# Optimization experiments

Hardware: AMD Instinct MI355X
Metric: run time of the kernel (lower is better)

The kernel has to match this reference:

```python
import jax, jax.numpy as jnp
import numpy as np

EPS = 1e-6      # l2_norm / denom clamp eps
BN_EPS = 1e-5   # BatchNorm eps


def _l2norm(x):
    # torch.norm(p=2, dim=-2, keepdim=True).clamp_min(eps)
    n = jnp.sqrt(jnp.sum(x * x, axis=-2, keepdims=True))
    return x / jnp.maximum(n, EPS)


def setup_inputs() -> dict:
    key = jax.random.key(0)
    ks = jax.random.split(key, 9)
    B, Cin_each, Co, H, W = 4, 256, 256, 128, 128
    Cq = Co // 8  # in_places // scale
    Cin = 4 * Cin_each
    return {
        "s5": jax.random.normal(ks[0], (B, Cin_each, H, W), jnp.float32),
        "s4": jax.random.normal(ks[1], (B, Cin_each, H, W), jnp.float32),
        "s3": jax.random.normal(ks[2], (B, Cin_each, H, W), jnp.float32),
        "s2": jax.random.normal(ks[3], (B, Cin_each, H, W), jnp.float32),
        # ConvBnRelu: 1x1 conv (no bias) + BN affine params
        "w_conv": jax.random.normal(ks[4], (Co, Cin), jnp.float32) * 0.03,
        "bn_gamma": jnp.ones((Co,), jnp.float32),
        "bn_beta": jnp.zeros((Co,), jnp.float32),
        # Attention 1x1 convs (with bias)
        "wq": jax.random.normal(ks[5], (Cq, Co), jnp.float32) * 0.06,
        "bq": jnp.zeros((Cq,), jnp.float32),
        "wk": jax.random.normal(ks[6], (Cq, Co), jnp.float32) * 0.06,
        "bk": jnp.zeros((Cq,), jnp.float32),
        "wv": jax.random.normal(ks[7], (Co, Co), jnp.float32) * 0.06,
        "bv": jnp.zeros((Co,), jnp.float32),
        # gamma is Parameter(zeros(1)) in the source; set nonzero so the
        # attention branch contributes to the output for kernel testing.
        "gamma": jnp.array(0.5, jnp.float32),
    }


def reference(s5, s4, s3, s2, w_conv, bn_gamma, bn_beta,
              wq, bq, wk, bk, wv, bv, gamma):
    # --- ConvBnRelu (1x1 conv, train-mode BN, ReLU) ---
    fcat = jnp.concatenate([s5, s4, s3, s2], axis=1)            # [B, 4C, H, W]
    x = jnp.einsum('oc,bchw->bohw', w_conv, fcat)               # 1x1 conv
    mu = x.mean(axis=(0, 2, 3), keepdims=True)
    var = x.var(axis=(0, 2, 3), keepdims=True)                  # biased, as torch BN
    x = (x - mu) / jnp.sqrt(var + BN_EPS)
    x = x * bn_gamma[None, :, None, None] + bn_beta[None, :, None, None]
    feat = jax.nn.relu(x)                                       # [B, C, H, W]

    # --- linear Attention (L2-norm QK, KV trick, no softmax) ---
    B, C, H, W = feat.shape
    N = H * W
    X = feat.reshape(B, C, N)
    Q = jnp.einsum('qc,bcn->bqn', wq, X) + bq[None, :, None]    # [B, Cq, N]
    K = jnp.einsum('qc,bcn->bqn', wk, X) + bk[None, :, None]    # [B, Cq, N]
    V = jnp.einsum('oc,bcn->bon', wv, X) + bv[None, :, None]    # [B, C, N]

    Qn = _l2norm(Q)                                             # norm over channel dim
    Kn = _l2norm(K)

    # denom: N + Q . sum_n K
    e = jnp.einsum('bqn,bq->bn', Qn, Kn.sum(axis=-1))           # [B, N]
    tailor = 1.0 / jnp.maximum(jnp.asarray(N, Qn.dtype) + e, 1e-6)

    # KV trick: [B, Cq, C] then project back through Q
    matrix = jnp.einsum('bqn,bcn->bqc', Kn, V)                  # [B, Cq, C]
    matrix_sum = V.sum(axis=-1)[:, :, None] + \
        jnp.einsum('bqn,bqc->bcn', Qn, matrix)                  # [B, C, N]

    weight_value = matrix_sum * tailor[:, None, :]              # [B, C, N]
    out = gamma * weight_value.reshape(B, C, H, W)
    out = jnp.nan_to_num(out, nan=0.0, posinf=1.0, neginf=-1.0)

    return out + feat
```

## Files before the change

### kernel.cpp

```cpp
#include <hip/hip_runtime.h>

#define B_   4
#define CO   256
#define CIN  1024
#define CQ   32
#define HN   16384
#define NPIX 65536
#define NTOT ((size_t)B_ * CO * HN)

typedef unsigned short ushort_t;
typedef __attribute__((ext_vector_type(8))) short bf16x8;
typedef __attribute__((ext_vector_type(4))) float f32x4;

__device__ __forceinline__ unsigned bf16pair(float x, float y) {
    unsigned xu = __float_as_uint(x), yu = __float_as_uint(y);
    unsigned xr = (xu + 0x7FFFu + ((xu >> 16) & 1u)) >> 16;
    unsigned yr = (yu + 0x7FFFu + ((yu >> 16) & 1u)) >> 16;
    return xr | (yr << 16);
}
__device__ __forceinline__ ushort_t bf16of(float x) {
    unsigned u = __float_as_uint(x);
    return (ushort_t)((u + 0x7FFFu + ((u >> 16) & 1u)) >> 16);
}
__device__ __forceinline__ float bf2f(ushort_t h) {
    return __uint_as_float(((unsigned)h) << 16);
}
__device__ __forceinline__ void unpack8(uint4 u, float* f) {
    f[0] = __uint_as_float(u.x << 16); f[1] = __uint_as_float(u.x & 0xffff0000u);
    f[2] = __uint_as_float(u.y << 16); f[3] = __uint_as_float(u.y & 0xffff0000u);
    f[4] = __uint_as_float(u.z << 16); f[5] = __uint_as_float(u.z & 0xffff0000u);
    f[6] = __uint_as_float(u.w << 16); f[7] = __uint_as_float(u.w & 0xffff0000u);
}
__device__ __forceinline__ void async16(void* lds, const void* g) {
    __builtin_amdgcn_global_load_lds(
        (const __attribute__((address_space(1))) void*)g,
        (__attribute__((address_space(3))) void*)lds, 16, 0, 0);
}

__global__ __launch_bounds__(256) void wcvt(
    const float* __restrict__ w, const float* __restrict__ wq,
    const float* __restrict__ wk, const float* __restrict__ wv,
    ushort_t* __restrict__ w_bf, ushort_t* __restrict__ wqk_bf,
    ushort_t* __restrict__ wv_bf)
{
    int i = blockIdx.x * 256 + threadIdx.x;
    if (i < 262144) {
        w_bf[i] = bf16of(w[i]);
    } else if (i < 278528) {
        int l = i - 262144; int row = l >> 8, col = l & 255;
        float v = (row < 32) ? wq[row * 256 + col] : wk[(row - 32) * 256 + col];
        wqk_bf[l] = bf16of(v);
    } else {
        int l = i - 278528;
        wv_bf[l] = bf16of(wv[l]);
    }
}

__global__ __launch_bounds__(256) void conv_mfma3(
    const float* __restrict__ s5, const float* __restrict__ s4,
    const float* __restrict__ s3, const float* __restrict__ s2,
    const ushort_t* __restrict__ w_bf, ushort_t* __restrict__ xb)
{
    __shared__ ushort_t Aw[2][128 * 32];
    __shared__ ushort_t Bn[2][128 * 40];
    const int o0 = blockIdx.x * 128;
    const int n0 = blockIdx.y * 128;
    const int b  = blockIdx.z;
    const int tid = threadIdx.x;
    const int wave = tid >> 6, lane = tid & 63, l15 = lane & 15, quad = lane >> 4;
    const int wm = wave & 1, wn = wave >> 1;
    const int n_st = tid & 127;
    const int kqb  = tid >> 7;
    const int bswz = ((n_st >> 3) & 3) << 1;
    f32x4 acc[4][4] = {};
    float v[4][4];

    auto loadB = [&](int k0) {
        const float* base = (k0 < 256) ? s5 : (k0 < 512) ? s4
                          : (k0 < 768) ? s3 : s2;
        const float* sp = base + ((size_t)b * 256 + (k0 & 255)) * HN + n0 + n_st;
        #pragma unroll
        for (int i = 0; i < 4; ++i) {
            const float* cp = sp + (size_t)(kqb + 2 * i) * 4 * HN;
            #pragma unroll
            for (int j = 0; j < 4; ++j) v[i][j] = cp[(size_t)j * HN];
        }
    };
    auto storeB = [&](int bi) {
        ushort_t* Bp = Bn[bi];
        #pragma unroll
        for (int i = 0; i < 4; ++i) {
            int pos = (kqb + 2 * i) ^ bswz;
            uint2 u = make_uint2(bf16pair(v[i][0], v[i][1]),
                                 bf16pair(v[i][2], v[i][3]));
            *(uint2*)&Bp[n_st * 40 + pos * 4] = u;
        }
    };
    auto issueA = [&](int k0, int bi) {
        #pragma unroll
        for (int r = 0; r < 2; ++r) {
            int row  = r * 64 + wave * 16;
            int orow = row + (lane >> 2);
            const ushort_t* g = w_bf + (size_t)(o0 + orow) * CIN + k0
                                + (((lane & 3) ^ ((orow >> 1) & 3)) << 3);
            async16(&Aw[bi][row * 32], g);
        }
    };

    issueA(0, 0);
    loadB(0);
    storeB(0);

    int buf = 0;
    for (int k0 = 0; k0 < CIN; k0 += 32) {
        __syncthreads();
        const bool more = (k0 + 32 < CIN);
        if (more) { issueA(k0 + 32, buf ^ 1); loadB(k0 + 32); }
        bf16x8 af[4], bfv[4];
        #pragma unroll
        for (int tm = 0; tm < 4; ++tm) {
            int orow = wm * 64 + tm * 16 + l15;
            int pos  = quad ^ ((orow >> 1) & 3);
            af[tm] = *(const bf16x8*)&Aw[buf][orow * 32 + pos * 8];
        }
        #pragma unroll
        for (int tn = 0; tn < 4; ++tn) {
            int nl = wn * 64 + tn * 16 + l15;
            int p0 = (2 * quad) ^ (((nl >> 3) & 3) << 1);
            bfv[tn] = *(const bf16x8*)&Bn[buf][nl * 40 + p0 * 4];
        }
        #pragma unroll
        for (int tm = 0; tm < 4; ++tm)
            #pragma unroll
            for (int tn = 0; tn < 4; ++tn)
                acc[tm][tn] = __builtin_amdgcn_mfma_f32_16x16x32_bf16(
                    af[tm], bfv[tn], acc[tm][tn], 0, 0, 0);
        if (more) storeB(buf ^ 1);
        buf ^= 1;
    }
    #pragma unroll
    for (int tm = 0; tm < 4; ++tm)
        #pragma unroll
        for (int r = 0; r < 4; ++r) {
            int o = o0 + wm * 64 + tm * 16 + quad * 4 + r;
            size_t base = ((size_t)b * CO + o) * HN + n0;
            #pragma unroll
            for (int tn = 0; tn < 4; ++tn)
                xb[base + wn * 64 + tn * 16 + l15] = bf16of(acc[tm][tn][r]);
        }
}

__global__ __launch_bounds__(256) void bn_stats(
    const ushort_t* __restrict__ xb, float* __restrict__ accum)
{
    const int o = blockIdx.x, seg = blockIdx.y, tid = threadIdx.x;
    const int wave = tid >> 6, lane = tid & 63;
    float s = 0.f, ss = 0.f;
    for (int b = 0; b < B_; ++b) {
        const ushort_t* p = xb + ((size_t)(b * CO + o)) * HN + seg * 2048 + tid * 8;
        uint4 u = *(const uint4*)p;
        float f[8]; unpack8(u, f);
        #pragma unroll
        for (int j = 0; j < 8; ++j) { s += f[j]; ss += f[j] * f[j]; }
    }
    #pragma unroll
    for (int m = 1; m < 64; m <<= 1) { s += __shfl_xor(s, m); ss += __shfl_xor(ss, m); }
    __shared__ float shs[4], shss[4];
    if (lane == 0) { shs[wave] = s; shss[wave] = ss; }
    __syncthreads();
    if (tid == 0) {
        atomicAdd(&accum[o],       shs[0] + shs[1] + shs[2] + shs[3]);
        atomicAdd(&accum[256 + o], shss[0] + shss[1] + shss[2] + shss[3]);
    }
}

__global__ __launch_bounds__(256) void bn_finalize(
    const float* __restrict__ accum, const float* __restrict__ g,
    const float* __restrict__ bt, float* __restrict__ scale,
    float* __restrict__ shift)
{
    int o = threadIdx.x;
    float mu  = accum[o] / (float)NPIX;
    float var = accum[256 + o] / (float)NPIX - mu * mu;
    float sc  = g[o] * rsqrtf(var + 1e-5f);
    scale[o] = sc;
    shift[o] = bt[o] - mu * sc;
}

__global__ __launch_bounds__(256) void bnrelu_t(
    const ushort_t* __restrict__ xb, const float* __restrict__ scale,
    const float* __restrict__ shift, ushort_t* __restrict__ featT)
{
    __shared__ ushort_t sh[64 * 68];
    const int hn0 = blockIdx.x * 64, c0 = blockIdx.y * 64, b = blockIdx.z;
    const int tid = threadIdx.x;
    {
        int cl = tid >> 2, seg = tid & 3;
        float sc = scale[c0 + cl], sf = shift[c0 + cl];
        const ushort_t* src = xb + ((size_t)(b * CO + c0 + cl)) * HN + hn0 + seg * 16;
        #pragma unroll
        for (int h = 0; h < 2; ++h) {
            uint4 u = *(const uint4*)(src + h * 8);
            float f[8]; unpack8(u, f);
            #pragma unroll
            for (int j = 0; j < 8; ++j) {
                float v = fmaxf(fmaf(sc, f[j], sf), 0.f);
                sh[(seg * 16 + h * 8 + j) * 68 + cl] = bf16of(v);
            }
        }
    }
    __syncthreads();
    {
        int nl = tid >> 2, seg = tid & 3;
        size_t gn = (size_t)b * HN + hn0 + nl;
        ushort_t* dst = featT + gn * CO + c0 + seg * 16;
        #pragma unroll
        for (int j = 0; j < 4; ++j)
            *(uint2*)(dst + j * 4) = *(const uint2*)&sh[nl * 68 + seg * 16 + j * 4];
    }
}

__global__ __launch_bounds__(256) void qk_mfma(
    const ushort_t* __restrict__ featT, const ushort_t* __restrict__ wqk_bf,
    const float* __restrict__ bq, const float* __restrict__ bk,
    ushort_t* __restrict__ Qt, ushort_t* __restrict__ KtT,
    float* __restrict__ Ksum)
{
    __shared__ ushort_t At[128 * 32];
    __shared__ ushort_t Bt[64 * 32];
    const int n0 = blockIdx.x * 128;
    const int b  = n0 >> 14;
    const int hn0 = n0 & 16383;
    const int tid = threadIdx.x;
    const int wave = tid >> 6, lane = tid & 63, l15 = lane & 15, quad = lane >> 4;
    const int nsub = (wave & 1) * 64;
    const int isK  = wave >> 1;
    f32x4 acc[4][2] = {};

    for (int k0 = 0; k0 < CO; k0 += 32) {
        #pragma unroll
        for (int r = 0; r < 2; ++r) {
            int row = r * 64 + wave * 16;
            const ushort_t* g = featT + (size_t)(n0 + row + (lane >> 2)) * CO
                                + k0 + (lane & 3) * 8;
            async16(&At[row * 32], g);
        }
        {
            int row = wave * 16;
            const ushort_t* g = wqk_bf + (size_t)(row + (lane >> 2)) * CO
                                + k0 + (lane & 3) * 8;
            async16(&Bt[row * 32], g);
        }
        __syncthreads();
        bf16x8 af[4], bfv[2];
        #pragma unroll
        for (int tm = 0; tm < 4; ++tm)
            af[tm] = *(const bf16x8*)&At[(nsub + tm * 16 + l15) * 32 + quad * 8];
        #pragma unroll
        for (int tc = 0; tc < 2; ++tc)
            bfv[tc] = *(const bf16x8*)&Bt[(isK * 32 + tc * 16 + l15) * 32 + quad * 8];
        #pragma unroll
        for (int tm = 0; tm < 4; ++tm)
            #pragma unroll
            for (int tc = 0; tc < 2; ++tc)
                acc[tm][tc] = __builtin_amdgcn_mfma_f32_16x16x32_bf16(
                    af[tm], bfv[tc], acc[tm][tc], 0, 0, 0);
        __syncthreads();
    }
    const float bias0 = isK ? bk[l15]      : bq[l15];
    const float bias1 = isK ? bk[16 + l15] : bq[16 + l15];
    float ks0 = 0.f, ks1 = 0.f;
    #pragma unroll
    for (int tm = 0; tm < 4; ++tm)
        #pragma unroll
        for (int r = 0; r < 4; ++r) {
            float v0 = acc[tm][0][r] + bias0;
            float v1 = acc[tm][1][r] + bias1;
            float sq = v0 * v0 + v1 * v1;
            sq += __shfl_xor(sq, 1); sq += __shfl_xor(sq, 2);
            sq += __shfl_xor(sq, 4); sq += __shfl_xor(sq, 8);
            float inv = 1.f / fmaxf(sqrtf(sq), 1e-6f);
            v0 *= inv; v1 *= inv;
            if (isK) {
                int hn = hn0 + nsub + tm * 16 + quad * 4 + r;
                KtT[((size_t)(b * CQ + l15)) * HN + hn]      = bf16of(v0);
                KtT[((size_t)(b * CQ + 16 + l15)) * HN + hn] = bf16of(v1);
            } else {
                int n = n0 + nsub + tm * 16 + quad * 4 + r;
                Qt[(size_t)n * CQ + l15]      = bf16of(v0);
                Qt[(size_t)n * CQ + 16 + l15] = bf16of(v1);
            }
            ks0 += v0; ks1 += v1;
        }
    if (isK) {
        ks0 += __shfl_xor(ks0, 16); ks0 += __shfl_xor(ks0, 32);
        ks1 += __shfl_xor(ks1, 16); ks1 += __shfl_xor(ks1, 32);
        if (quad == 0) {
            atomicAdd(&Ksum[b * CQ + l15],      ks0);
            atomicAdd(&Ksum[b * CQ + 16 + l15], ks1);
        }
    }
}

__global__ __launch_bounds__(256) void v_kv_mfma(
    const ushort_t* __restrict__ featT, const ushort_t* __restrict__ wv_bf,
    const float* __restrict__ bv, const ushort_t* __restrict__ KtT,
    float* __restrict__ matT, float* __restrict__ Vsum)
{
    __shared__ ushort_t sh[128 * 136];
    ushort_t* At = sh;
    ushort_t* Bt = sh + 4096;
    const int n0  = blockIdx.x * 128;
    const int co0 = blockIdx.y * 128;
    const int b   = n0 >> 14;
    const int hn0 = n0 & 16383;
    const int tid = threadIdx.x;
    const int wave = tid >> 6, lane = tid & 63, l15 = lane & 15, quad = lane >> 4;
    const int wm = wave & 1, wn = wave >> 1;
    f32x4 acc[4][4] = {};

    for (int k0 = 0; k0 < CO; k0 += 32) {
        #pragma unroll
        for (int r = 0; r < 2; ++r) {
            int row = r * 64 + wave * 16;
            const ushort_t* ga = featT + (size_t)(n0 + row + (lane >> 2)) * CO
                                 + k0 + (lane & 3) * 8;
            async16(&At[row * 32], ga);
            const ushort_t* gb = wv_bf + (size_t)(co0 + row + (lane >> 2)) * CO
                                 + k0 + (lane & 3) * 8;
            async16(&Bt[row * 32], gb);
        }
        __syncthreads();
        bf16x8 af[4], bfv[4];
        #pragma unroll
        for (int tm = 0; tm < 4; ++tm)
            af[tm] = *(const bf16x8*)&At[(wm * 64 + tm * 16 + l15) * 32 + quad * 8];
        #pragma unroll
        for (int tn = 0; tn < 4; ++tn)
            bfv[tn] = *(const bf16x8*)&Bt[(wn * 64 + tn * 16 + l15) * 32 + quad * 8];
        #pragma unroll
        for (int tm = 0; tm < 4; ++tm)
            #pragma unroll
            for (int tn = 0; tn < 4; ++tn)
                acc[tm][tn] = __builtin_amdgcn_mfma_f32_16x16x32_bf16(
                    af[tm], bfv[tn], acc[tm][tn], 0, 0, 0);
        __syncthreads();
    }
    ushort_t* Vlds = sh;
    float bvl[4], vsum_p[4] = {};
    #pragma unroll
    for (int tn = 0; tn < 4; ++tn) bvl[tn] = bv[co0 + wn * 64 + tn * 16 + l15];
    #pragma unroll
    for (int tm = 0; tm < 4; ++tm)
        #pragma unroll
        for (int tn = 0; tn < 4; ++tn) {
            float x0 = acc[tm][tn][0] + bvl[tn];
            float x1 = acc[tm][tn][1] + bvl[tn];
            float x2 = acc[tm][tn][2] + bvl[tn];
            float x3 = acc[tm][tn][3] + bvl[tn];
            vsum_p[tn] += (x0 + x1) + (x2 + x3);
            uint2 u = make_uint2(bf16pair(x0, x1), bf16pair(x2, x3));
            int c_loc = wn * 64 + tn * 16 + l15;
            int nb    = wm * 64 + tm * 16 + quad * 4;
            *(uint2*)&Vlds[c_loc * 136 + nb] = u;
        }
    #pragma unroll
    for (int tn = 0; tn < 4; ++tn) {
        float s = vsum_p[tn];
        s += __shfl_xor(s, 16); s += __shfl_xor(s, 32);
        if (quad == 0)
            atomicAdd(&Vsum[b * CO + co0 + wn * 64 + tn * 16 + l15], s);
    }
    __syncthreads();
    f32x4 acc2[2][2] = {};
    #pragma unroll
    for (int ks = 0; ks < 4; ++ks) {
        bf16x8 a2[2], b2[2];
        #pragma unroll
        for (int t2 = 0; t2 < 2; ++t2)
            a2[t2] = *(const bf16x8*)&Vlds[(wave * 32 + t2 * 16 + l15) * 136
                                           + ks * 32 + quad * 8];
        #pragma unroll
        for (int tc = 0; tc < 2; ++tc)
            b2[tc] = *(const bf16x8*)&KtT[((size_t)(b * CQ + tc * 16 + l15)) * HN
                                          + hn0 + ks * 32 + quad * 8];
        #pragma unroll
        for (int t2 = 0; t2 < 2; ++t2)
            #pragma unroll
            for (int tc = 0; tc < 2; ++tc)
                acc2[t2][tc] = __builtin_amdgcn_mfma_f32_16x16x32_bf16(
                    a2[t2], b2[tc], acc2[t2][tc], 0, 0, 0);
    }
    #pragma unroll
    for (int t2 = 0; t2 < 2; ++t2)
        #pragma unroll
        for (int tc = 0; tc < 2; ++tc)
            #pragma unroll
            for (int r = 0; r < 4; ++r) {
                int c = co0 + wave * 32 + t2 * 16 + quad * 4 + r;
                atomicAdd(&matT[b * 8192 + c * CQ + tc * 16 + l15],
                          acc2[t2][tc][r]);
            }
}

__global__ __launch_bounds__(256) void tailor_k(
    const ushort_t* __restrict__ Qt, const float* __restrict__ Ksum,
    float* __restrict__ tailor)
{
    __shared__ float ks[CQ];
    const int n = blockIdx.x * 256 + threadIdx.x;
    const int b = n >> 14;
    if (threadIdx.x < CQ) ks[threadIdx.x] = Ksum[b * CQ + threadIdx.x];
    __syncthreads();
    const uint4* q = (const uint4*)&Qt[(size_t)n * CQ];
    float e = 0.f;
    #pragma unroll
    for (int i = 0; i < 4; ++i) {
        float f[8]; unpack8(q[i], f);
        #pragma unroll
        for (int j = 0; j < 8; ++j) e += f[j] * ks[i * 8 + j];
    }
    tailor[n] = 1.f / fmaxf((float)HN + e, 1e-6f);
}

__global__ __launch_bounds__(256) void final_mfma(
    const ushort_t* __restrict__ xb, const ushort_t* __restrict__ Qt,
    const float* __restrict__ matT, const float* __restrict__ Vsum,
    const float* __restrict__ tailor, const float* __restrict__ scale,
    const float* __restrict__ shift, const float* __restrict__ gamma_p,
    float* __restrict__ out)
{
    const int c0 = blockIdx.x * 128;
    const int n0 = blockIdx.y * 128;
    const int b  = n0 >> 14, hn0 = n0 & 16383;
    const int tid = threadIdx.x;
    const int wave = tid >> 6, lane = tid & 63, l15 = lane & 15, quad = lane >> 4;
    const int wm = wave & 1, wn = wave >> 1;
    const float gamma = gamma_p[0];

    bf16x8 af[4], bfv[4];
    #pragma unroll
    for (int tm = 0; tm < 4; ++tm) {
        int c = c0 + wm * 64 + tm * 16 + l15;
        const float* mp = matT + b * 8192 + c * CQ + quad * 8;
        float4 m0 = *(const float4*)mp;
        float4 m1 = *(const float4*)(mp + 4);
        union { bf16x8 v; unsigned u[4]; } t;
        t.u[0] = bf16pair(m0.x, m0.y); t.u[1] = bf16pair(m0.z, m0.w);
        t.u[2] = bf16pair(m1.x, m1.y); t.u[3] = bf16pair(m1.z, m1.w);
        af[tm] = t.v;
    }
    #pragma unroll
    for (int tn = 0; tn < 4; ++tn) {
        int n = n0 + wn * 64 + tn * 16 + l15;
        bfv[tn] = *(const bf16x8*)&Qt[(size_t)n * CQ + quad * 8];
    }
    f32x4 acc[4][4] = {};
    #pragma unroll
    for (int tm = 0; tm < 4; ++tm)
        #pragma unroll
        for (int tn = 0; tn < 4; ++tn)
            acc[tm][tn] = __builtin_amdgcn_mfma_f32_16x16x32_bf16(
                af[tm], bfv[tn], acc[tm][tn], 0, 0, 0);

    float tl[4];
    #pragma unroll
    for (int tn = 0; tn < 4; ++tn) tl[tn] = tailor[n0 + wn * 64 + tn * 16 + l15];

    #pragma unroll
    for (int tm = 0; tm < 4; ++tm)
        #pragma unroll
        for (int r = 0; r < 4; ++r) {
            int c = c0 + wm * 64 + tm * 16 + quad * 4 + r;
            float vs = Vsum[b * CO + c];
            float sc = scale[c], sf = shift[c];
            size_t rowbase = ((size_t)(b * CO + c)) * HN + hn0;
            #pragma unroll
            for (int tn = 0; tn < 4; ++tn) {
                int nl = wn * 64 + tn * 16 + l15;
                float val = gamma * (acc[tm][tn][r] + vs) * tl[tn];
                if (isnan(val)) val = 0.f;
                else if (isinf(val)) val = (val > 0.f) ? 1.f : -1.f;
                float feat = fmaxf(fmaf(sc, bf2f(xb[rowbase + nl]), sf), 0.f);
                out[rowbase + nl] = val + feat;
            }
        }
}

extern "C" void kernel_launch(void* const* d_in, const int* in_sizes, int n_in,
                              void* d_out, int out_size, void* d_ws, size_t ws_size,
                              hipStream_t stream)
{
    const float* s5      = (const float*)d_in[0];
    const float* s4      = (const float*)d_in[1];
    const float* s3      = (const float*)d_in[2];
    const float* s2      = (const float*)d_in[3];
    const float* w_conv  = (const float*)d_in[4];
    const float* bn_g    = (const float*)d_in[5];
    const float* bn_b    = (const float*)d_in[6];
    const float* wq      = (const float*)d_in[7];
    const float* bq      = (const float*)d_in[8];
    const float* wk      = (const float*)d_in[9];
    const float* bk      = (const float*)d_in[10];
    const float* wv      = (const float*)d_in[11];
    const float* bv      = (const float*)d_in[12];
    const float* gamma_p = (const float*)d_in[13];

    char* p = (char*)d_ws;
    ushort_t* xb     = (ushort_t*)p;  p += NTOT * 2;
    ushort_t* featT  = (ushort_t*)p;  p += NTOT * 2;
    ushort_t* Qt     = (ushort_t*)p;  p += (size_t)NPIX * CQ * 2;
    ushort_t* KtT    = (ushort_t*)p;  p += (size_t)NPIX * CQ * 2;
    ushort_t* w_bf   = (ushort_t*)p;  p += (size_t)CO * CIN * 2;
    ushort_t* wqk_bf = (ushort_t*)p;  p += 64 * CO * 2;
    ushort_t* wv_bf  = (ushort_t*)p;  p += (size_t)CO * CO * 2;
    float* matT  = (float*)p;
    float* Ksum  = matT + (size_t)B_ * CO * CQ;
    float* Vsum  = Ksum + B_ * CQ;
    float* accum = Vsum + B_ * CO;
    size_t zero_bytes = (size_t)(32768 + 128 + 1024 + 512) * 4;
    p += zero_bytes;
    float* scale  = (float*)p;  p += 256 * 4;
    float* shift  = (float*)p;  p += 256 * 4;
    float* tailor = (float*)p;  p += (size_t)NPIX * 4;

    hipMemsetAsync(matT, 0, zero_bytes, stream);
    wcvt<<<1344, 256, 0, stream>>>(w_conv, wq, wk, wv, w_bf, wqk_bf, wv_bf);
    conv_mfma3<<<dim3(2, 128, B_), 256, 0, stream>>>(s5, s4, s3, s2, w_bf, xb);
    bn_stats<<<dim3(256, 8), 256, 0, stream>>>(xb, accum);
    bn_finalize<<<1, 256, 0, stream>>>(accum, bn_g, bn_b, scale, shift);
    bnrelu_t<<<dim3(256, 4, B_), 256, 0, stream>>>(xb, scale, shift, featT);
    qk_mfma<<<512, 256, 0, stream>>>(featT, wqk_bf, bq, bk, Qt, KtT, Ksum);
    tailor_k<<<256, 256, 0, stream>>>(Qt, Ksum, tailor);
    v_kv_mfma<<<dim3(512, 2), 256, 0, stream>>>(featT, wv_bf, bv, KtT, matT, Vsum);
    final_mfma<<<dim3(2, 512), 256, 0, stream>>>(xb, Qt, matT, Vsum, tailor,
                                                 scale, shift, gamma_p,
                                                 (float*)d_out);
}
```

Baseline: 422.5 us.

## Fuse BN statistics into conv epilogue and stage epilogue stores through LDS

The BatchNorm sum and sum-of-squares reductions move into the conv GEMM epilogue, computed from fp32 accumulators with shuffles and atomics, which removes the separate bn_stats pass that re-read the bf16 conv output. The conv and final kernels now stage their output tiles through shared memory so global stores (and the xb reads in the final kernel) are 16-byte vectorized and coalesced. The conv main loop is also reordered to store B before a raw barrier. Statistics now come from fp32 rather than bf16-rounded values, and the epilogues gain extra barriers and shared-memory traffic.

```diff
diff --git a/kernel.cpp b/kernel.cpp
--- a/kernel.cpp
+++ b/kernel.cpp
@@ -56,10 +56,11 @@
     }
 }
 
-__global__ __launch_bounds__(256) void conv_mfma3(
+__global__ __launch_bounds__(256) void conv_mfma4(
     const float* __restrict__ s5, const float* __restrict__ s4,
     const float* __restrict__ s3, const float* __restrict__ s2,
-    const ushort_t* __restrict__ w_bf, ushort_t* __restrict__ xb)
+    const ushort_t* __restrict__ w_bf, ushort_t* __restrict__ xb,
+    float* __restrict__ accum)
 {
     __shared__ ushort_t Aw[2][128 * 32];
     __shared__ ushort_t Bn[2][128 * 40];
@@ -109,13 +110,14 @@
 
     issueA(0, 0);
     loadB(0);
-    storeB(0);
 
     int buf = 0;
     for (int k0 = 0; k0 < CIN; k0 += 32) {
-        __syncthreads();
-        const bool more = (k0 + 32 < CIN);
-        if (more) { issueA(k0 + 32, buf ^ 1); loadB(k0 + 32); }
+        storeB(buf);
+        asm volatile("s_waitcnt lgkmcnt(0)" ::: "memory");
+        __builtin_amdgcn_s_barrier();
+        __builtin_amdgcn_sched_barrier(0);
+        if (k0 + 32 < CIN) { issueA(k0 + 32, buf ^ 1); loadB(k0 + 32); }
         bf16x8 af[4], bfv[4];
         #pragma unroll
         for (int tm = 0; tm < 4; ++tm) {
@@ -135,42 +137,50 @@
             for (int tn = 0; tn < 4; ++tn)
                 acc[tm][tn] = __builtin_amdgcn_mfma_f32_16x16x32_bf16(
                     af[tm], bfv[tn], acc[tm][tn], 0, 0, 0);
-        if (more) storeB(buf ^ 1);
         buf ^= 1;
     }
+
     #pragma unroll
     for (int tm = 0; tm < 4; ++tm)
         #pragma unroll
         for (int r = 0; r < 4; ++r) {
-            int o = o0 + wm * 64 + tm * 16 + quad * 4 + r;
-            size_t base = ((size_t)b * CO + o) * HN + n0;
+            float s = 0.f, ss = 0.f;
+            #pragma unroll
+            for (int tn = 0; tn < 4; ++tn) {
+                float x = acc[tm][tn][r];
+                s += x; ss += x * x;
+            }
+            s += __shfl_xor(s, 1); ss += __shfl_xor(ss, 1);
+            s += __shfl_xor(s, 2); ss += __shfl_xor(ss, 2);
+            s += __shfl_xor(s, 4); ss += __shfl_xor(ss, 4);
+            s += __shfl_xor(s, 8); ss += __shfl_xor(ss, 8);
+            if (l15 == 0) {
+                int o = o0 + wm * 64 + tm * 16 + quad * 4 + r;
+                atomicAdd(&accum[o], s);
+                atomicAdd(&accum[256 + o], ss);
+            }
+        }
+
+    ushort_t* st = Bn[0];
+    const int orow = tid >> 3, oseg = tid & 7;
+    #pragma unroll
+    for (int tm = 0; tm < 4; ++tm) {
+        if (tm) __syncthreads();
+        #pragma unroll
+        for (int r = 0; r < 4; ++r) {
+            int row = wm * 16 + quad * 4 + r;
             #pragma unroll
             for (int tn = 0; tn < 4; ++tn)
-                xb[base + wn * 64 + tn * 16 + l15] = bf16of(acc[tm][tn][r]);
-        }
-}
-
-__global__ __launch_bounds__(256) void bn_stats(
-    const ushort_t* __restrict__ xb, float* __restrict__ accum)
-{
-    const int o = blockIdx.x, seg = blockIdx.y, tid = threadIdx.x;
-    const int wave = tid >> 6, lane = tid & 63;
-    float s = 0.f, ss = 0.f;
-    for (int b = 0; b < B_; ++b) {
-        const ushort_t* p = xb + ((size_t)(b * CO + o)) * HN + seg * 2048 + tid * 8;
-        uint4 u = *(const uint4*)p;
-        float f[8]; unpack8(u, f);
-        #pragma unroll
-        for (int j = 0; j < 8; ++j) { s += f[j]; ss += f[j] * f[j]; }
-    }
-    #pragma unroll
-    for (int m = 1; m < 64; m <<= 1) { s += __shfl_xor(s, m); ss += __shfl_xor(ss, m); }
-    __shared__ float shs[4], shss[4];
-    if (lane == 0) { shs[wave] = s; shss[wave] = ss; }
-    __syncthreads();
-    if (tid == 0) {
-        atomicAdd(&accum[o],       shs[0] + shs[1] + shs[2] + shs[3]);
-        atomicAdd(&accum[256 + o], shss[0] + shss[1] + shss[2] + shss[3]);
+                st[row * 136 + wn * 64 + tn * 16 + l15] = bf16of(acc[tm][tn][r]);
+        }
+        __syncthreads();
+        {
+            int c = o0 + (orow >> 4) * 64 + tm * 16 + (orow & 15);
+            size_t base = ((size_t)(b * CO + c)) * HN + n0 + oseg * 16;
+            const uint4* sp = (const uint4*)&st[orow * 136 + oseg * 16];
+            *(uint4*)(xb + base)     = sp[0];
+            *(uint4*)(xb + base + 8) = sp[1];
+        }
     }
 }
 
@@ -430,6 +440,7 @@
     const float* __restrict__ shift, const float* __restrict__ gamma_p,
     float* __restrict__ out)
 {
+    __shared__ float sh[32 * 132];
     const int c0 = blockIdx.x * 128;
     const int n0 = blockIdx.y * 128;
     const int b  = n0 >> 14, hn0 = n0 & 16383;
@@ -467,24 +478,48 @@
     #pragma unroll
     for (int tn = 0; tn < 4; ++tn) tl[tn] = tailor[n0 + wn * 64 + tn * 16 + l15];
 
-    #pragma unroll
-    for (int tm = 0; tm < 4; ++tm)
+    const int orow = tid >> 3, oseg = tid & 7;
+    #pragma unroll
+    for (int tm = 0; tm < 4; ++tm) {
+        if (tm) __syncthreads();
         #pragma unroll
         for (int r = 0; r < 4; ++r) {
             int c = c0 + wm * 64 + tm * 16 + quad * 4 + r;
             float vs = Vsum[b * CO + c];
-            float sc = scale[c], sf = shift[c];
-            size_t rowbase = ((size_t)(b * CO + c)) * HN + hn0;
+            int row = wm * 16 + quad * 4 + r;
             #pragma unroll
             for (int tn = 0; tn < 4; ++tn) {
-                int nl = wn * 64 + tn * 16 + l15;
                 float val = gamma * (acc[tm][tn][r] + vs) * tl[tn];
                 if (isnan(val)) val = 0.f;
                 else if (isinf(val)) val = (val > 0.f) ? 1.f : -1.f;
-                float feat = fmaxf(fmaf(sc, bf2f(xb[rowbase + nl]), sf), 0.f);
-                out[rowbase + nl] = val + feat;
-            }
-        }
+                sh[row * 132 + wn * 64 + tn * 16 + l15] = val;
+            }
+        }
+        __syncthreads();
+        {
+            int c = c0 + (orow >> 4) * 64 + tm * 16 + (orow & 15);
+            float sc = scale[c], sf = shift[c];
+            size_t base = ((size_t)(b * CO + c)) * HN + hn0 + oseg * 16;
+            const float* sp = &sh[orow * 132 + oseg * 16];
+            const uint4* xp = (const uint4*)(xb + base);
+            #pragma unroll
+            for (int h = 0; h < 2; ++h) {
+                uint4 u = xp[h];
+                float f[8]; unpack8(u, f);
+                float4 q0, q1;
+                q0.x = sp[h * 8 + 0] + fmaxf(fmaf(sc, f[0], sf), 0.f);
+                q0.y = sp[h * 8 + 1] + fmaxf(fmaf(sc, f[1], sf), 0.f);
+                q0.z = sp[h * 8 + 2] + fmaxf(fmaf(sc, f[2], sf), 0.f);
+                q0.w = sp[h * 8 + 3] + fmaxf(fmaf(sc, f[3], sf), 0.f);
+                q1.x = sp[h * 8 + 4] + fmaxf(fmaf(sc, f[4], sf), 0.f);
+                q1.y = sp[h * 8 + 5] + fmaxf(fmaf(sc, f[5], sf), 0.f);
+                q1.z = sp[h * 8 + 6] + fmaxf(fmaf(sc, f[6], sf), 0.f);
+                q1.w = sp[h * 8 + 7] + fmaxf(fmaf(sc, f[7], sf), 0.f);
+                *(float4*)(out + base + h * 8)     = q0;
+                *(float4*)(out + base + h * 8 + 4) = q1;
+            }
+        }
+    }
 }
 
 extern "C" void kernel_launch(void* const* d_in, const int* in_sizes, int n_in,
@@ -526,8 +561,8 @@
 
     hipMemsetAsync(matT, 0, zero_bytes, stream);
     wcvt<<<1344, 256, 0, stream>>>(w_conv, wq, wk, wv, w_bf, wqk_bf, wv_bf);
-    conv_mfma3<<<dim3(2, 128, B_), 256, 0, stream>>>(s5, s4, s3, s2, w_bf, xb);
-    bn_stats<<<dim3(256, 8), 256, 0, stream>>>(xb, accum);
+    conv_mfma4<<<dim3(2, 128, B_), 256, 0, stream>>>(s5, s4, s3, s2, w_bf, xb,
+                                                     accum);
     bn_finalize<<<1, 256, 0, stream>>>(accum, bn_g, bn_b, scale, shift);
     bnrelu_t<<<dim3(256, 4, B_), 256, 0, stream>>>(xb, scale, shift, featT);
     qk_mfma<<<512, 256, 0, stream>>>(featT, wqk_bf, bq, bk, Qt, KtT, Ksum);
```

New measurement: 479.9 us. 1.14x slower.
